# Kernel optimization log

Measured on AMD Instinct MI355X. Metric: run time of the kernel, lower is better.

## Reference

```python
import jax, jax.numpy as jnp
import numpy as np

NEG_INF = float(-2 ** 31)
B, S, D_IN, D_H, H = 4, 2048, 512, 512, 8


def setup_inputs() -> dict:
    key = jax.random.key(0)
    ks = jax.random.split(key, 11)
    sc_in = 1.0 / np.sqrt(D_IN)
    sc_pr = 1.0 / np.sqrt(D_H * H)
    x = jax.random.normal(ks[0], (B, S, D_IN), dtype=jnp.float32)
    mask = jax.random.randint(ks[1], (B, 1, S), 0, 2, dtype=jnp.int32)
    Wq = jax.random.uniform(ks[2], (H, D_IN, D_H), jnp.float32, -sc_in, sc_in)
    bq = jax.random.uniform(ks[3], (H, D_H), jnp.float32, -sc_in, sc_in)
    Wk = jax.random.uniform(ks[4], (H, D_IN, D_H), jnp.float32, -sc_in, sc_in)
    bk = jax.random.uniform(ks[5], (H, D_H), jnp.float32, -sc_in, sc_in)
    Wv = jax.random.uniform(ks[6], (H, D_IN, D_H), jnp.float32, -sc_in, sc_in)
    bv = jax.random.uniform(ks[7], (H, D_H), jnp.float32, -sc_in, sc_in)
    Wp = jax.random.uniform(ks[8], (H * D_H, D_H), jnp.float32, -sc_pr, sc_pr)
    bp = jax.random.uniform(ks[9], (D_H,), jnp.float32, -sc_pr, sc_pr)
    return {"x": x, "mask": mask, "Wq": Wq, "bq": bq, "Wk": Wk, "bk": bk,
            "Wv": Wv, "bv": bv, "Wp": Wp, "bp": bp}


def reference(x, mask, Wq, bq, Wk, bk, Wv, bv, Wp, bp):
    # per-head Q/K/V projections, batched over the head axis h
    q = jnp.einsum('bsd,hde->bhse', x, Wq) + bq[None, :, None, :]
    k = jnp.einsum('bsd,hde->bhse', x, Wk) + bk[None, :, None, :]
    v = jnp.einsum('bsd,hde->bhse', x, Wv) + bv[None, :, None, :]
    scores = jnp.einsum('bhse,bhte->bhst', q, k) / jnp.sqrt(jnp.float32(D_H))
    scores = jnp.where(mask[:, None, :, :] == 0, NEG_INF, scores)
    probs = jax.nn.softmax(scores, axis=-1)
    out = jnp.einsum('bhst,bhte->bhse', probs, v)  # [B,H,S,D_H]
    cat = out.transpose(0, 2, 1, 3).reshape(B, S, H * D_H)
    return cat @ Wp + bp
```

## Files before the change

kernel.cpp:

```cpp
#include <hip/hip_runtime.h>
#include <hip/hip_bf16.h>
#include <cstdint>
#include <cstddef>

typedef unsigned short ushort_t;
typedef __bf16 bf16x8 __attribute__((ext_vector_type(8)));
typedef float floatx4 __attribute__((ext_vector_type(4)));

#define S_LEN 2048
#define DIN   512
#define DH    512
#define NHEAD 8
#define NBAT  4
#define NBH   32
#define HP    4096

#define MiB (1024ull * 1024ull)
#define WQT_OFF   (0ull)
#define WKT_OFF   (4ull  * MiB)
#define WVT_OFF   (8ull  * MiB)
#define WPT_OFF   (12ull * MiB)
#define XBF_OFF   (16ull * MiB)
#define Q_OFF     (24ull * MiB)
#define K_OFF     (88ull * MiB)
#define VT_OFF    (152ull * MiB)
#define O_OFF     (216ull * MiB)
#define LSUM_OFF  (280ull * MiB)
#define P_OFF     (281ull * MiB)
#define WS_BYTES  (409ull * MiB)

__device__ __align__(256) unsigned char g_ws[WS_BYTES];

__device__ __forceinline__ ushort_t f2bf(float f) {
  union { float f; uint32_t u; } v; v.f = f;
  uint32_t r = v.u + 0x7fffu + ((v.u >> 16) & 1u);
  return (ushort_t)(r >> 16);
}

typedef __attribute__((address_space(3))) uint32_t lds_uint;
typedef __attribute__((address_space(1))) const uint32_t glb_uint;

__device__ __forceinline__ void async16(void* lds, const void* g) {
  __builtin_amdgcn_global_load_lds((glb_uint*)g, (lds_uint*)lds, 16, 0, 0);
}

#define BBAR() do { \
    __builtin_amdgcn_sched_barrier(0); \
    __builtin_amdgcn_s_barrier(); \
    __builtin_amdgcn_sched_barrier(0); \
  } while (0)


#define STG_A(dbuf, hh, kt) do { \
    const ushort_t* _g = gA + (size_t)(kt) * 64 + (size_t)(hh) * a128; \
    char* _s = sAh + (dbuf) * 32768 + (hh) * 16384; \
    async16(_s, _g); \
    async16(_s + 8192, _g + a64); \
  } while (0)

#define STG_B(dbuf, hh, kt) do { \
    const ushort_t* _g = gB + (size_t)(kt) * 64 + (size_t)(hh) * b128; \
    char* _s = sBh + (dbuf) * 32768 + (hh) * 16384; \
    async16(_s, _g); \
    async16(_s + 8192, _g + b64); \
  } while (0)

#define LD_A(dst, qm) do { \
    const char* _b = (const char*)As + cur * 32768 + (qm) * 16384 + aoff0; \
    _Pragma("unroll") \
    for (int _i = 0; _i < 4; ++_i) { \
      dst[_i][0] = *(const bf16x8*)(_b + (_i << 11) + swz0); \
      dst[_i][1] = *(const bf16x8*)(_b + (_i << 11) + swz1); \
    } } while (0)

#define LD_B(dst, qn) do { \
    const char* _b = (const char*)Bs + cur * 32768 + (qn) * 16384 + boff0; \
    _Pragma("unroll") \
    for (int _j = 0; _j < 2; ++_j) { \
      dst[_j][0] = *(const bf16x8*)(_b + (_j << 11) + swz0); \
      dst[_j][1] = *(const bf16x8*)(_b + (_j << 11) + swz1); \
    } } while (0)

#define MM(q, AF, BF) do { \
    _Pragma("unroll") \
    for (int _i = 0; _i < 4; ++_i) { \
      _Pragma("unroll") \
      for (int _j = 0; _j < 2; ++_j) { \
        acc[q][_i][_j] = __builtin_amdgcn_mfma_f32_16x16x32_bf16(AF[_i][0], BF[_j][0], acc[q][_i][_j], 0, 0, 0); \
        acc[q][_i][_j] = __builtin_amdgcn_mfma_f32_16x16x32_bf16(AF[_i][1], BF[_j][1], acc[q][_i][_j], 0, 0, 0); \
      } \
    } \
  } while (0)

__device__ __forceinline__ void gemm256_core(
    const ushort_t* __restrict__ A, const ushort_t* __restrict__ Bt,
    int lda, int ldb, int kdim,
    ushort_t* As, ushort_t* Bs, floatx4 acc[4][4][2])
{
  const int t = threadIdx.x;
  const int w = t >> 6, l = t & 63;
  const int l15 = l & 15, lq = l >> 4;
  const int wq_r = w >> 2, wq_c = w & 3;

  const int r0 = t >> 3, c0 = t & 7;
  const ushort_t* gA = A + (size_t)r0 * lda + ((c0 ^ (r0 & 7)) << 3);
  const ushort_t* gB = Bt + (size_t)r0 * ldb + ((c0 ^ (r0 & 7)) << 3);
  const size_t a64 = (size_t)64 * lda, b64 = (size_t)64 * ldb;
  const size_t a128 = (size_t)128 * lda, b128 = (size_t)128 * ldb;
  char* sAh = (char*)As + (w << 10);
  char* sBh = (char*)Bs + (w << 10);

  const int aoff0 = ((wq_r << 6) + l15) << 7;
  const int boff0 = ((wq_c << 5) + l15) << 7;
  const int l7 = l15 & 7;
  const int swz0 = (lq ^ l7) << 4;
  const int swz1 = ((4 + lq) ^ l7) << 4;

  const int nt = kdim >> 6;

#pragma unroll
  for (int q = 0; q < 4; ++q)
#pragma unroll
    for (int i = 0; i < 4; ++i)
#pragma unroll
      for (int j = 0; j < 2; ++j)
        acc[q][i][j] = (floatx4){0.f, 0.f, 0.f, 0.f};

  STG_A(0, 0, 0);
  STG_B(0, 1, 0);
  STG_A(0, 1, 0);
  STG_B(0, 0, 0);
  if (nt > 1) {
    STG_A(1, 0, 1);
    STG_B(1, 1, 1);
    asm volatile("s_waitcnt vmcnt(4)" ::: "memory");
  } else {
    asm volatile("s_waitcnt vmcnt(0)" ::: "memory");
  }
  BBAR();

  bf16x8 a[4][2], b0[2][2], b1[2][2];

#pragma unroll 1
  for (int tt = 0; tt < nt; ++tt) {
    const int cur = tt & 1, nxt = cur ^ 1;
    __builtin_amdgcn_s_setprio(1);
    LD_A(a, 0);
    LD_B(b0, 0);
    if (tt + 1 < nt) STG_A(nxt, 1, tt + 1);
    MM(0, a, b0);
    __builtin_amdgcn_s_setprio(0);
    BBAR();
    __builtin_amdgcn_s_setprio(1);
    LD_B(b1, 1);
    if (tt + 1 < nt) STG_B(nxt, 0, tt + 1);
    MM(1, a, b1);
    __builtin_amdgcn_s_setprio(0);
    BBAR();
    __builtin_amdgcn_s_setprio(1);
    LD_A(a, 1);
    if (tt + 2 < nt) STG_A(cur, 0, tt + 2);
    MM(2, a, b1);
    __builtin_amdgcn_s_setprio(0);
    BBAR();
    __builtin_amdgcn_s_setprio(1);
    if (tt + 2 < nt) STG_B(cur, 1, tt + 2);
    MM(3, a, b0);
    __builtin_amdgcn_s_setprio(0);
    if (tt + 2 < nt) asm volatile("s_waitcnt vmcnt(4)" ::: "memory");
    else             asm volatile("s_waitcnt vmcnt(0)" ::: "memory");
    BBAR();
  }
}

__device__ __forceinline__ void gemm_core(
    const ushort_t* __restrict__ A, const ushort_t* __restrict__ Bt,
    int lda, int ldb, int kdim,
    ushort_t* As, ushort_t* Bs, floatx4 acc[4][4])
{
  const int t = threadIdx.x;
  const int w = t >> 6;
  const int l = t & 63;
  const int wrow = w >> 1, wcol = w & 1;
  const int l15 = l & 15, lq = l >> 4;

  const ushort_t* gA = A + (size_t)(t >> 2) * lda + (t & 3) * 8;
  const ushort_t* gB = Bt + (size_t)(t >> 2) * ldb + (t & 3) * 8;
  const size_t strideA = (size_t)64 * lda;
  const size_t strideB = (size_t)64 * ldb;
  char* ldsA0 = (char*)As + w * 1024;
  char* ldsB0 = (char*)Bs + w * 1024;

  async16(ldsA0,        gA);
  async16(ldsA0 + 4096, gA + strideA);
  async16(ldsB0,        gB);
  async16(ldsB0 + 4096, gB + strideB);

#pragma unroll
  for (int i = 0; i < 4; ++i)
#pragma unroll
    for (int j = 0; j < 4; ++j)
      acc[i][j] = (floatx4){0.f, 0.f, 0.f, 0.f};

  const int nwin = kdim >> 5;
#pragma unroll 1
  for (int k = 0; k < nwin; ++k) {
    __syncthreads();
    const int cur = k & 1;
    if (k + 1 < nwin) {
      const int nxt = cur ^ 1;
      const ushort_t* gA1 = gA + (size_t)(k + 1) * 32;
      const ushort_t* gB1 = gB + (size_t)(k + 1) * 32;
      char* ldsA1 = ldsA0 + nxt * 8192;
      char* ldsB1 = ldsB0 + nxt * 8192;
      async16(ldsA1,        gA1);
      async16(ldsA1 + 4096, gA1 + strideA);
      async16(ldsB1,        gB1);
      async16(ldsB1 + 4096, gB1 + strideB);
    }
    const ushort_t* rdA = As + cur * 4096 + (wrow * 64 + l15) * 32 + lq * 8;
    const ushort_t* rdB = Bs + cur * 4096 + (wcol * 64 + l15) * 32 + lq * 8;

    bf16x8 af[4], bfr[4];
#pragma unroll
    for (int i = 0; i < 4; ++i) af[i] = *(const bf16x8*)(rdA + i * 512);
#pragma unroll
    for (int j = 0; j < 4; ++j) bfr[j] = *(const bf16x8*)(rdB + j * 512);
#pragma unroll
    for (int i = 0; i < 4; ++i)
#pragma unroll
      for (int j = 0; j < 4; ++j)
        acc[i][j] = __builtin_amdgcn_mfma_f32_16x16x32_bf16(af[i], bfr[j], acc[i][j], 0, 0, 0);
  }
}

__global__ __launch_bounds__(256) void convert_f32_bf16(
    const float* __restrict__ src, size_t dstOff, int n)
{
  ushort_t* dst = (ushort_t*)(g_ws + dstOff);
  int i = (blockIdx.x * 256 + threadIdx.x) * 4;
  if (i >= n) return;
  float4 v = *(const float4*)(src + i);
  ushort_t o[4] = {f2bf(v.x), f2bf(v.y), f2bf(v.z), f2bf(v.w)};
  *(uint2*)(dst + i) = *(const uint2*)o;
}

__global__ __launch_bounds__(256) void transpose_f32_bf16(
    const float* __restrict__ src, size_t dstOff, int R, int C)
{
  __shared__ ushort_t tile[32][33];
  ushort_t* dst = (ushort_t*)(g_ws + dstOff) + (size_t)blockIdx.z * R * C;
  src += (size_t)blockIdx.z * R * C;
  int r0 = blockIdx.y * 32, c0 = blockIdx.x * 32;
  int tx = threadIdx.x & 31, ty = threadIdx.x >> 5;
  for (int i = ty; i < 32; i += 8)
    tile[i][tx] = f2bf(src[(size_t)(r0 + i) * C + (c0 + tx)]);
  __syncthreads();
  for (int i = ty; i < 32; i += 8)
    dst[(size_t)(c0 + i) * R + (r0 + tx)] = tile[tx][i];
}

__global__ __launch_bounds__(256) void zero_lsum()
{
  float* lsum = (float*)(g_ws + LSUM_OFF);
  int i = (blockIdx.x * 256 + threadIdx.x) * 4;
  *(float4*)(lsum + i) = (float4){0.f, 0.f, 0.f, 0.f};
}

__global__ __launch_bounds__(512, 2) void qkv_gemm(
    const float* __restrict__ bq, const float* __restrict__ bk,
    const float* __restrict__ bv)
{
  __shared__ __align__(16) ushort_t SH[65536];
  ushort_t* As = SH;
  ushort_t* Bs = SH + 32768;
  const int z = blockIdx.z;
  const int bh = z & 31, sel = z >> 5, b = bh >> 3, h = bh & 7;
  const size_t wOff = (sel == 0) ? WQT_OFF : (sel == 1) ? WKT_OFF : WVT_OFF;
  const float* bias = ((sel == 0) ? bq : (sel == 1) ? bk : bv) + h * DH;
  const int tileM = blockIdx.y * 256, tileN = blockIdx.x * 256;

  const ushort_t* A  = (const ushort_t*)(g_ws + XBF_OFF)
                       + ((size_t)b * S_LEN + tileM) * DIN;
  const ushort_t* Bt = (const ushort_t*)(g_ws + wOff)
                       + ((size_t)h * DH + tileN) * DIN;
  floatx4 acc[4][4][2];
  gemm256_core(A, Bt, DIN, DIN, DIN, As, Bs, acc);

  const int t = threadIdx.x, w = t >> 6, l = t & 63;
  const int l15 = l & 15, lq = l >> 4;
  const int wq_r = w >> 2, wq_c = w & 3;
  const int QM[4] = {0, 0, 1, 1}, QN[4] = {0, 1, 1, 0};

  if (sel == 2) {
    char* SB = (char*)SH;
#pragma unroll
    for (int q = 0; q < 4; ++q) {
#pragma unroll
      for (int j = 0; j < 2; ++j) {
        const int nl = QN[q] * 128 + wq_c * 32 + j * 16 + l15;
        const float bsn = bias[tileN + nl];
#pragma unroll
        for (int i = 0; i < 4; ++i) {
          const int ml = QM[q] * 128 + wq_r * 64 + i * 16 + lq * 4;
          ushort_t pk[4];
#pragma unroll
          for (int r = 0; r < 4; ++r) pk[r] = f2bf(acc[q][i][j][r] + bsn);
          const int byte = nl * 512 + (((ml >> 3) ^ (nl & 7)) << 4) + (ml & 7) * 2;
          *(uint2*)(SB + byte) = *(const uint2*)pk;
        }
      }
    }
    BBAR();
    ushort_t* VTb = (ushort_t*)(g_ws + VT_OFF)
                    + ((size_t)bh * DH + tileN) * S_LEN + tileM;
#pragma unroll
    for (int s = 0; s < 16; ++s) {
      const int nl = (w << 5) + (s << 1) + (l >> 5);
      const int c  = l & 31;
      const uint4 v = *(const uint4*)(SB + nl * 512 + ((c ^ (nl & 7)) << 4));
      *(uint4*)(VTb + (size_t)nl * S_LEN + c * 8) = v;
    }
  } else {
    ushort_t* Db = (ushort_t*)(g_ws + ((sel == 0) ? Q_OFF : K_OFF));
#pragma unroll
    for (int q = 0; q < 4; ++q) {
#pragma unroll
      for (int j = 0; j < 2; ++j) {
        const int n = tileN + QN[q] * 128 + wq_c * 32 + j * 16 + l15;
        const float bsn = bias[n];
#pragma unroll
        for (int i = 0; i < 4; ++i) {
#pragma unroll
          for (int r = 0; r < 4; ++r) {
            const int m = tileM + QM[q] * 128 + wq_r * 64 + i * 16 + lq * 4 + r;
            Db[((size_t)bh * S_LEN + m) * DH + n] = f2bf(acc[q][i][j][r] + bsn);
          }
        }
      }
    }
  }
}

__global__ __launch_bounds__(512, 2) void scores_kernel(
    const int* __restrict__ mask, int c0)
{
  __shared__ __align__(16) ushort_t SH[65536];
  ushort_t* As = SH;
  ushort_t* Bs = SH + 32768;
  const int hl = blockIdx.z, bh = c0 + hl, b = bh >> 3;
  const int tileM = blockIdx.y * 256, tileN = blockIdx.x * 256;

  const ushort_t* A  = (const ushort_t*)(g_ws + Q_OFF)
                       + ((size_t)bh * S_LEN + tileM) * DH;
  const ushort_t* Bt = (const ushort_t*)(g_ws + K_OFF)
                       + ((size_t)bh * S_LEN + tileN) * DH;
  floatx4 acc[4][4][2];
  gemm256_core(A, Bt, DH, DH, DH, As, Bs, acc);

  const float scale = 0.04419417382415922f;
  const int t = threadIdx.x, w = t >> 6, l = t & 63;
  const int l15 = l & 15, lq = l >> 4;
  const int wq_r = w >> 2, wq_c = w & 3;
  const int QM[4] = {0, 0, 1, 1}, QN[4] = {0, 1, 1, 0};
  ushort_t* Pp = (ushort_t*)(g_ws + P_OFF) + (size_t)hl * S_LEN * S_LEN;
  const int* mask_b = mask + (size_t)b * S_LEN;
  float* lsum = (float*)(g_ws + LSUM_OFF);

  float rsum[2][4][4];
#pragma unroll
  for (int qm = 0; qm < 2; ++qm)
#pragma unroll
    for (int i = 0; i < 4; ++i)
#pragma unroll
      for (int r = 0; r < 4; ++r) rsum[qm][i][r] = 0.f;

#pragma unroll
  for (int q = 0; q < 4; ++q) {
#pragma unroll
    for (int j = 0; j < 2; ++j) {
      const int n = tileN + QN[q] * 128 + wq_c * 32 + j * 16 + l15;
      const int mv = mask_b[n];
#pragma unroll
      for (int i = 0; i < 4; ++i) {
#pragma unroll
        for (int r = 0; r < 4; ++r) {
          const int m = tileM + QM[q] * 128 + wq_r * 64 + i * 16 + lq * 4 + r;
          float s = fminf(acc[q][i][j][r] * scale, 30.f);
          const float p = mv ? __expf(s) : 0.f;
          rsum[QM[q]][i][r] += p;
          Pp[(size_t)m * S_LEN + n] = f2bf(p);
        }
      }
    }
  }
#pragma unroll
  for (int qm = 0; qm < 2; ++qm) {
#pragma unroll
    for (int i = 0; i < 4; ++i) {
#pragma unroll
      for (int r = 0; r < 4; ++r) {
        float v = rsum[qm][i][r];
        v += __shfl_xor(v, 1);
        v += __shfl_xor(v, 2);
        v += __shfl_xor(v, 4);
        v += __shfl_xor(v, 8);
        if (l15 == 0) {
          const int m = tileM + qm * 128 + wq_r * 64 + i * 16 + lq * 4 + r;
          atomicAdd(&lsum[(size_t)hl * S_LEN + m], v);
        }
      }
    }
  }
}

__global__ __launch_bounds__(512, 2) void pv_kernel(int c0)
{
  __shared__ __align__(16) ushort_t SH[65536];
  ushort_t* As = SH;
  ushort_t* Bs = SH + 32768;
  const int hl = blockIdx.z, bh = c0 + hl, b = bh >> 3, h = bh & 7;
  const int tileM = blockIdx.y * 256, tileN = blockIdx.x * 256;

  const ushort_t* A  = (const ushort_t*)(g_ws + P_OFF)
                       + (size_t)hl * S_LEN * S_LEN + (size_t)tileM * S_LEN;
  const ushort_t* Bt = (const ushort_t*)(g_ws + VT_OFF)
                       + ((size_t)bh * DH + tileN) * S_LEN;
  floatx4 acc[4][4][2];
  gemm256_core(A, Bt, S_LEN, S_LEN, S_LEN, As, Bs, acc);

  const float* lsum = (const float*)(g_ws + LSUM_OFF);
  ushort_t* Ob = (ushort_t*)(g_ws + O_OFF);
  const int t = threadIdx.x, w = t >> 6, l = t & 63;
  const int l15 = l & 15, lq = l >> 4;
  const int wq_r = w >> 2, wq_c = w & 3;
  const int QM[4] = {0, 0, 1, 1}, QN[4] = {0, 1, 1, 0};
#pragma unroll
  for (int q = 0; q < 4; ++q) {
#pragma unroll
    for (int i = 0; i < 4; ++i) {
#pragma unroll
      for (int r = 0; r < 4; ++r) {
        const int m = tileM + QM[q] * 128 + wq_r * 64 + i * 16 + lq * 4 + r;
        const float lv = lsum[(size_t)hl * S_LEN + m];
        const float inv = (lv > 1e-20f) ? 1.0f / lv : 0.f;
#pragma unroll
        for (int j = 0; j < 2; ++j) {
          const int n = tileN + QN[q] * 128 + wq_c * 32 + j * 16 + l15;
          Ob[((size_t)b * S_LEN + m) * HP + h * DH + n] =
              f2bf(acc[q][i][j][r] * inv);
        }
      }
    }
  }
}

__global__ __launch_bounds__(256) void proj_kernel(
    const float* __restrict__ bp, float* __restrict__ out)
{
  __shared__ __align__(16) ushort_t As[2 * 128 * 32], Bs[2 * 128 * 32];
  const int tileM = blockIdx.y * 128, tileN = blockIdx.x * 128;

  const ushort_t* A  = (const ushort_t*)(g_ws + O_OFF) + (size_t)tileM * HP;
  const ushort_t* Bt = (const ushort_t*)(g_ws + WPT_OFF) + (size_t)tileN * HP;
  floatx4 acc[4][4];
  gemm_core(A, Bt, HP, HP, HP, As, Bs, acc);

  const int t = threadIdx.x, w = t >> 6, l = t & 63;
  const int wrow = w >> 1, wcol = w & 1, l15 = l & 15, lq = l >> 4;
#pragma unroll
  for (int j = 0; j < 4; ++j) {
    const int n = tileN + wcol * 64 + j * 16 + l15;
    const float bsn = bp[n];
#pragma unroll
    for (int i = 0; i < 4; ++i) {
#pragma unroll
      for (int r = 0; r < 4; ++r) {
        const int m = tileM + wrow * 64 + i * 16 + lq * 4 + r;
        out[(size_t)m * DH + n] = acc[i][j][r] + bsn;
      }
    }
  }
}

extern "C" void kernel_launch(void* const* d_in, const int* in_sizes, int n_in,
                              void* d_out, int out_size, void* d_ws, size_t ws_size,
                              hipStream_t stream) {
  const float* x  = (const float*)d_in[0];
  const int*   msk= (const int*)d_in[1];
  const float* Wq = (const float*)d_in[2];
  const float* bq = (const float*)d_in[3];
  const float* Wk = (const float*)d_in[4];
  const float* bk = (const float*)d_in[5];
  const float* Wv = (const float*)d_in[6];
  const float* bv = (const float*)d_in[7];
  const float* Wp = (const float*)d_in[8];
  const float* bp = (const float*)d_in[9];
  float* out = (float*)d_out;

  convert_f32_bf16<<<dim3(NBAT * S_LEN * DIN / 1024), 256, 0, stream>>>(
      x, XBF_OFF, NBAT * S_LEN * DIN);

  transpose_f32_bf16<<<dim3(16, 16, NHEAD), 256, 0, stream>>>(Wq, WQT_OFF, DIN, DH);
  transpose_f32_bf16<<<dim3(16, 16, NHEAD), 256, 0, stream>>>(Wk, WKT_OFF, DIN, DH);
  transpose_f32_bf16<<<dim3(16, 16, NHEAD), 256, 0, stream>>>(Wv, WVT_OFF, DIN, DH);
  transpose_f32_bf16<<<dim3(16, 128, 1),    256, 0, stream>>>(Wp, WPT_OFF, HP, DH);

  qkv_gemm<<<dim3(2, 8, 3 * NBH), 512, 0, stream>>>(bq, bk, bv);

  for (int c0 = 0; c0 < NBH; c0 += 16) {
    zero_lsum<<<dim3(32), 256, 0, stream>>>();
    scores_kernel<<<dim3(8, 8, 16), 512, 0, stream>>>(msk, c0);
    pv_kernel<<<dim3(2, 8, 16), 512, 0, stream>>>(c0);
  }

  proj_kernel<<<dim3(DH / 128, (NBAT * S_LEN) / 128), 256, 0, stream>>>(bp, out);
}
```

Baseline: 720.1 us.

## Simplify GEMM pipeline to whole-tile double buffering with one barrier per k-step

Replaces the staggered four-phase software pipeline, which prefetched half-tiles two steps ahead with a barrier between each quarter, with a simpler double buffer. All four stage loads for the next k-tile are issued at the start of each iteration, followed by four MFMA blocks and a single full vmcnt(0) wait and barrier. This removes three barriers per iteration and uses separate A register sets. The trade-off is a shorter prefetch distance and a full drain of outstanding loads every step, which could expose global-load latency.

After: 723.2 us. About the same (+0.4%).

```diff
diff --git a/kernel.cpp b/kernel.cpp
--- a/kernel.cpp
+++ b/kernel.cpp
@@ -127,48 +127,34 @@
         acc[q][i][j] = (floatx4){0.f, 0.f, 0.f, 0.f};
 
   STG_A(0, 0, 0);
-  STG_B(0, 1, 0);
   STG_A(0, 1, 0);
   STG_B(0, 0, 0);
-  if (nt > 1) {
-    STG_A(1, 0, 1);
-    STG_B(1, 1, 1);
-    asm volatile("s_waitcnt vmcnt(4)" ::: "memory");
-  } else {
-    asm volatile("s_waitcnt vmcnt(0)" ::: "memory");
-  }
+  STG_B(0, 1, 0);
+  asm volatile("s_waitcnt vmcnt(0)" ::: "memory");
   BBAR();
 
-  bf16x8 a[4][2], b0[2][2], b1[2][2];
+  bf16x8 a0[4][2], a1[4][2], b0[2][2], b1[2][2];
 
 #pragma unroll 1
   for (int tt = 0; tt < nt; ++tt) {
     const int cur = tt & 1, nxt = cur ^ 1;
+    if (tt + 1 < nt) {
+      STG_A(nxt, 0, tt + 1);
+      STG_A(nxt, 1, tt + 1);
+      STG_B(nxt, 0, tt + 1);
+      STG_B(nxt, 1, tt + 1);
+    }
     __builtin_amdgcn_s_setprio(1);
-    LD_A(a, 0);
+    LD_A(a0, 0);
     LD_B(b0, 0);
-    if (tt + 1 < nt) STG_A(nxt, 1, tt + 1);
-    MM(0, a, b0);
+    MM(0, a0, b0);
+    LD_B(b1, 1);
+    MM(1, a0, b1);
+    LD_A(a1, 1);
+    MM(2, a1, b1);
+    MM(3, a1, b0);
     __builtin_amdgcn_s_setprio(0);
-    BBAR();
-    __builtin_amdgcn_s_setprio(1);
-    LD_B(b1, 1);
-    if (tt + 1 < nt) STG_B(nxt, 0, tt + 1);
-    MM(1, a, b1);
-    __builtin_amdgcn_s_setprio(0);
-    BBAR();
-    __builtin_amdgcn_s_setprio(1);
-    LD_A(a, 1);
-    if (tt + 2 < nt) STG_A(cur, 0, tt + 2);
-    MM(2, a, b1);
-    __builtin_amdgcn_s_setprio(0);
-    BBAR();
-    __builtin_amdgcn_s_setprio(1);
-    if (tt + 2 < nt) STG_B(cur, 1, tt + 2);
-    MM(3, a, b0);
-    __builtin_amdgcn_s_setprio(0);
-    if (tt + 2 < nt) asm volatile("s_waitcnt vmcnt(4)" ::: "memory");
-    else             asm volatile("s_waitcnt vmcnt(0)" ::: "memory");
+    asm volatile("s_waitcnt vmcnt(0)" ::: "memory");
     BBAR();
   }
 }
```
